# Kernel optimization log

Measured on AMD Instinct MI355X. Metric: run time of the kernel, lower is better.

Reference implementation:

```python
import jax, jax.numpy as jnp
import numpy as np

DT_RANK = 160
D_STATE = 16


def setup_inputs() -> dict:
    key = jax.random.key(0)
    ks = jax.random.split(key, 13)
    B, D, E = 32, 2560, 5120
    s = lambda k, shape, sc=0.02: (jax.random.normal(k, shape, dtype=jnp.float32) * sc)
    return {
        "x": jax.random.normal(ks[0], (1, 1, B, D), dtype=jnp.float32),
        "W_in_ssm": s(ks[1], (D, E)),
        "W_in_mlp": s(ks[2], (D, E)),
        "W_out": s(ks[3], (E, D)),
        "conv_w": s(ks[4], (4, B, E), 0.1),
        "conv_b": s(ks[5], (B, E), 0.1),
        "conv_states": jax.random.normal(ks[6], (3, 1, 1, B, E), dtype=jnp.float32),
        "Wx": s(ks[7], (E, DT_RANK + 2 * D_STATE)),
        "W_dt": s(ks[8], (DT_RANK, E)),
        "dt_bias": s(ks[9], (E,), 0.5),
        "A_log": jax.random.uniform(ks[10], (E, D_STATE), dtype=jnp.float32),
        "D": s(ks[11], (E,), 1.0),
        "h": jax.random.normal(ks[12], (B, E, D_STATE), dtype=jnp.float32) * 0.1,
    }


def reference(x, W_in_ssm, W_in_mlp, W_out, conv_w, conv_b, conv_states, Wx, W_dt, dt_bias, A_log, D, h):
    # x: [1,1,B,d_model]
    x_ssm = x @ W_in_ssm  # [1,1,B,E]
    # FIFO: 3 carried conv states + newest projection -> 4 taps
    states = jnp.concatenate([conv_states, x_ssm[None]], axis=0)  # [4,1,1,B,E]
    # unrolled 4-tap causal depthwise conv (per-batch-broadcast weights) + bias + SiLU
    conv = jnp.einsum('tabne,tne->abne', states, conv_w) + conv_b  # [1,1,B,E]
    conv = jax.nn.silu(conv)

    # --- single-step selective SSM (Mamba decode) ---
    xt = conv[0, 0]  # [B,E]
    dbc = xt @ Wx  # [B, dt_rank + 2*d_state]
    dt = jax.nn.softplus(dbc[:, :DT_RANK] @ W_dt + dt_bias)  # [B,E]
    Bm = dbc[:, DT_RANK:DT_RANK + D_STATE]  # [B,N]
    Cm = dbc[:, DT_RANK + D_STATE:]         # [B,N]
    A = -jnp.exp(A_log)                      # [E,N]
    dA = jnp.exp(dt[:, :, None] * A[None])   # [B,E,N]
    h_new = h * dA + (dt[:, :, None] * Bm[:, None, :]) * xt[:, :, None]
    y = jnp.einsum('ben,bn->be', h_new, Cm) + D * xt  # [B,E]
    y = y[None, None]  # [1,1,B,E]

    # gated residual branch: silu-activated mlp projection
    residual = jax.nn.silu(x @ W_in_mlp)  # [1,1,B,E]
    out = y * residual
    return out @ W_out  # [1,1,B,d_model]
```

## Files before the change

### kernel.cpp

```cpp
#include <hip/hip_runtime.h>
#include <math.h>

#define EE 5120
#define DD 2560
#define BB 32

__global__ __launch_bounds__(256) void k0_prep(const float* __restrict__ x,
                                               float* __restrict__ xT,
                                               float* __restrict__ dbc) {
  int g = blockIdx.x * 256 + threadIdx.x;
  if (g < BB * DD) {
    int b = g / DD, k = g % DD;
    xT[k * BB + b] = x[g];
  }
  if (g < BB * 192) dbc[g] = 0.f;
}

__global__ __launch_bounds__(256) void k1a_gemm_in(const float* __restrict__ Wssm,
                                                   const float* __restrict__ Wmlp,
                                                   const float* __restrict__ xT,
                                                   float* __restrict__ P1) {
  const int bid  = blockIdx.x;
  const int cb   = bid % 160;
  const int so   = bid / 160;
  const int lane = threadIdx.x & 63;
  const int ks   = __builtin_amdgcn_readfirstlane((int)(threadIdx.x >> 6));
  const int c    = cb * 64 + lane;
  const float* __restrict__ W = (c < EE) ? Wssm : Wmlp;
  const int e  = (c < EE) ? c : c - EE;
  const int k0 = so * 320 + ks * 80;

  float acc[BB];
#pragma unroll
  for (int b = 0; b < BB; ++b) acc[b] = 0.f;

  const float* __restrict__ wp = W + (size_t)k0 * EE + e;
  const float* __restrict__ xp = xT + k0 * BB;
  for (int kk = 0; kk < 80; kk += 4) {
    float w0 = wp[(size_t)(kk + 0) * EE];
    float w1 = wp[(size_t)(kk + 1) * EE];
    float w2 = wp[(size_t)(kk + 2) * EE];
    float w3 = wp[(size_t)(kk + 3) * EE];
#pragma unroll
    for (int b = 0; b < BB; ++b) acc[b] = fmaf(xp[(kk + 0) * BB + b], w0, acc[b]);
#pragma unroll
    for (int b = 0; b < BB; ++b) acc[b] = fmaf(xp[(kk + 1) * BB + b], w1, acc[b]);
#pragma unroll
    for (int b = 0; b < BB; ++b) acc[b] = fmaf(xp[(kk + 2) * BB + b], w2, acc[b]);
#pragma unroll
    for (int b = 0; b < BB; ++b) acc[b] = fmaf(xp[(kk + 3) * BB + b], w3, acc[b]);
  }

  __shared__ float red[4][64][17];
  const int ksid = threadIdx.x >> 6;
#pragma unroll
  for (int half = 0; half < 2; ++half) {
    __syncthreads();
#pragma unroll
    for (int i = 0; i < 16; ++i) red[ksid][lane][i] = acc[half * 16 + i];
    __syncthreads();
#pragma unroll
    for (int j = 0; j < 4; ++j) {
      int bi = ksid * 4 + j;
      float v = red[0][lane][bi] + red[1][lane][bi] +
                red[2][lane][bi] + red[3][lane][bi];
      int b = half * 16 + bi;
      P1[((size_t)(so * BB + b)) * 10240 + c] = v;
    }
  }
}

__global__ __launch_bounds__(256) void k1b_epilogue(const float* __restrict__ P1,
                                                    const float* __restrict__ cs,
                                                    const float* __restrict__ cw,
                                                    const float* __restrict__ cbv,
                                                    float* __restrict__ xt,
                                                    float* __restrict__ res) {
  int g = blockIdx.x * 256 + threadIdx.x;
  int e = g % EE;
  int b = g / EE;
  float xs = 0.f, xm = 0.f;
#pragma unroll
  for (int so = 0; so < 8; ++so) {
    xs += P1[((size_t)(so * BB + b)) * 10240 + e];
    xm += P1[((size_t)(so * BB + b)) * 10240 + EE + e];
  }
  size_t be = (size_t)b * EE + e;
  const size_t T = (size_t)BB * EE;
  float conv = cs[be] * cw[be] + cs[T + be] * cw[T + be] +
               cs[2 * T + be] * cw[2 * T + be] + xs * cw[3 * T + be] + cbv[be];
  float sig = 1.f / (1.f + expf(-conv));
  xt[be] = conv * sig;
  float sm = 1.f / (1.f + expf(-xm));
  res[be] = xm * sm;
}

__global__ __launch_bounds__(256) void k2_dbc(const float* __restrict__ xt,
                                              const float* __restrict__ Wx,
                                              float* __restrict__ dbc) {
  const int bid  = blockIdx.x;
  const int cbi  = bid % 3;
  const int so   = bid / 3;
  const int lane = threadIdx.x & 63;
  const int j    = cbi * 64 + lane;
  const int k0   = so * 80 + (int)(threadIdx.x >> 6) * 20;

  float acc[BB];
#pragma unroll
  for (int b = 0; b < BB; ++b) acc[b] = 0.f;

  for (int kk = 0; kk < 20; kk += 4) {
    int k = k0 + kk;
    float w0 = Wx[(size_t)(k + 0) * 192 + j];
    float w1 = Wx[(size_t)(k + 1) * 192 + j];
    float w2 = Wx[(size_t)(k + 2) * 192 + j];
    float w3 = Wx[(size_t)(k + 3) * 192 + j];
#pragma unroll
    for (int b = 0; b < BB; ++b) acc[b] = fmaf(xt[(size_t)b * EE + k + 0], w0, acc[b]);
#pragma unroll
    for (int b = 0; b < BB; ++b) acc[b] = fmaf(xt[(size_t)b * EE + k + 1], w1, acc[b]);
#pragma unroll
    for (int b = 0; b < BB; ++b) acc[b] = fmaf(xt[(size_t)b * EE + k + 2], w2, acc[b]);
#pragma unroll
    for (int b = 0; b < BB; ++b) acc[b] = fmaf(xt[(size_t)b * EE + k + 3], w3, acc[b]);
  }

  __shared__ float red[4][64][17];
  const int ksid = threadIdx.x >> 6;
#pragma unroll
  for (int half = 0; half < 2; ++half) {
    __syncthreads();
#pragma unroll
    for (int i = 0; i < 16; ++i) red[ksid][lane][i] = acc[half * 16 + i];
    __syncthreads();
#pragma unroll
    for (int jj = 0; jj < 4; ++jj) {
      int bi = ksid * 4 + jj;
      float v = red[0][lane][bi] + red[1][lane][bi] +
                red[2][lane][bi] + red[3][lane][bi];
      int b = half * 16 + bi;
      atomicAdd(&dbc[b * 192 + j], v);
    }
  }
}

__global__ __launch_bounds__(256) void k3_ssm(const float* __restrict__ dbc,
                                              const float* __restrict__ Wdt,
                                              const float* __restrict__ dt_bias,
                                              const float* __restrict__ A_log,
                                              const float* __restrict__ Dvec,
                                              const float* __restrict__ h,
                                              const float* __restrict__ xt,
                                              const float* __restrict__ res,
                                              float* __restrict__ zT) {
  const int eb   = blockIdx.x % 80;
  const int bg   = blockIdx.x / 80;
  const int lane = threadIdx.x & 63;
  const int sub  = __builtin_amdgcn_readfirstlane((int)(threadIdx.x >> 6));
  const int e    = eb * 64 + lane;
  const int bq   = bg * 4 + sub;
  const int b0   = bq * 2, b1 = b0 + 1;

  float a0 = 0.f, a1 = 0.f;
  const float* __restrict__ d0 = dbc + b0 * 192;
  const float* __restrict__ d1 = dbc + b1 * 192;
  for (int r = 0; r < 160; r += 4) {
    float w0 = Wdt[(size_t)(r + 0) * EE + e];
    float w1 = Wdt[(size_t)(r + 1) * EE + e];
    float w2 = Wdt[(size_t)(r + 2) * EE + e];
    float w3 = Wdt[(size_t)(r + 3) * EE + e];
    a0 = fmaf(d0[r + 0], w0, a0);  a1 = fmaf(d1[r + 0], w0, a1);
    a0 = fmaf(d0[r + 1], w1, a0);  a1 = fmaf(d1[r + 1], w1, a1);
    a0 = fmaf(d0[r + 2], w2, a0);  a1 = fmaf(d1[r + 2], w2, a1);
    a0 = fmaf(d0[r + 3], w3, a0);  a1 = fmaf(d1[r + 3], w3, a1);
  }

  float An[16];
#pragma unroll
  for (int n = 0; n < 16; ++n) An[n] = -expf(A_log[e * 16 + n]);
  const float bias = dt_bias[e];
  const float Dv = Dvec[e];

#pragma unroll
  for (int t = 0; t < 2; ++t) {
    int b = t ? b1 : b0;
    float a = t ? a1 : a0;
    float v = a + bias;
    float dt = (v > 20.f) ? v : log1pf(expf(v));
    size_t be = (size_t)b * EE + e;
    float xb = xt[be];
    const float* __restrict__ hb = h + be * 16;
    const float* __restrict__ Bm = dbc + b * 192 + 160;
    const float* __restrict__ Cm = dbc + b * 192 + 176;
    float y = 0.f;
#pragma unroll
    for (int n = 0; n < 16; ++n) {
      float dA = expf(dt * An[n]);
      float hn = fmaf(hb[n], dA, dt * Bm[n] * xb);
      y = fmaf(hn, Cm[n], y);
    }
    y = fmaf(Dv, xb, y);
    zT[e * BB + b] = y * res[be];
  }
}

__global__ __launch_bounds__(256) void k4a_gemm_out(const float* __restrict__ Wout,
                                                    const float* __restrict__ zT,
                                                    float* __restrict__ P4) {
  const int bid  = blockIdx.x;
  const int cb   = bid % 40;
  const int so   = bid / 40;
  const int lane = threadIdx.x & 63;
  const int ks   = __builtin_amdgcn_readfirstlane((int)(threadIdx.x >> 6));
  const int d    = cb * 64 + lane;
  const int k0   = so * 320 + ks * 80;

  float acc[BB];
#pragma unroll
  for (int b = 0; b < BB; ++b) acc[b] = 0.f;

  const float* __restrict__ wp = Wout + (size_t)k0 * DD + d;
  const float* __restrict__ xp = zT + k0 * BB;
  for (int kk = 0; kk < 80; kk += 4) {
    float w0 = wp[(size_t)(kk + 0) * DD];
    float w1 = wp[(size_t)(kk + 1) * DD];
    float w2 = wp[(size_t)(kk + 2) * DD];
    float w3 = wp[(size_t)(kk + 3) * DD];
#pragma unroll
    for (int b = 0; b < BB; ++b) acc[b] = fmaf(xp[(kk + 0) * BB + b], w0, acc[b]);
#pragma unroll
    for (int b = 0; b < BB; ++b) acc[b] = fmaf(xp[(kk + 1) * BB + b], w1, acc[b]);
#pragma unroll
    for (int b = 0; b < BB; ++b) acc[b] = fmaf(xp[(kk + 2) * BB + b], w2, acc[b]);
#pragma unroll
    for (int b = 0; b < BB; ++b) acc[b] = fmaf(xp[(kk + 3) * BB + b], w3, acc[b]);
  }

  __shared__ float red[4][64][17];
  const int ksid = threadIdx.x >> 6;
#pragma unroll
  for (int half = 0; half < 2; ++half) {
    __syncthreads();
#pragma unroll
    for (int i = 0; i < 16; ++i) red[ksid][lane][i] = acc[half * 16 + i];
    __syncthreads();
#pragma unroll
    for (int j = 0; j < 4; ++j) {
      int bi = ksid * 4 + j;
      float v = red[0][lane][bi] + red[1][lane][bi] +
                red[2][lane][bi] + red[3][lane][bi];
      int b = half * 16 + bi;
      P4[((size_t)(so * BB + b)) * DD + d] = v;
    }
  }
}

__global__ __launch_bounds__(256) void k4b_reduce(const float* __restrict__ P4,
                                                  float* __restrict__ out) {
  int g = blockIdx.x * 256 + threadIdx.x;
  int d = g % DD;
  int b = g / DD;
  float s = 0.f;
#pragma unroll
  for (int so = 0; so < 16; ++so) s += P4[((size_t)(so * BB + b)) * DD + d];
  out[g] = s;
}

extern "C" void kernel_launch(void* const* d_in, const int* in_sizes, int n_in,
                              void* d_out, int out_size, void* d_ws, size_t ws_size,
                              hipStream_t stream) {
  const float* x       = (const float*)d_in[0];
  const float* Wssm    = (const float*)d_in[1];
  const float* Wmlp    = (const float*)d_in[2];
  const float* Wout    = (const float*)d_in[3];
  const float* conv_w  = (const float*)d_in[4];
  const float* conv_b  = (const float*)d_in[5];
  const float* conv_st = (const float*)d_in[6];
  const float* Wx      = (const float*)d_in[7];
  const float* Wdt     = (const float*)d_in[8];
  const float* dt_bias = (const float*)d_in[9];
  const float* A_log   = (const float*)d_in[10];
  const float* Dvec    = (const float*)d_in[11];
  const float* h       = (const float*)d_in[12];
  float* out = (float*)d_out;

  float* ws = (float*)d_ws;
  float* xT  = ws;
  float* P1  = xT  + 81920;
  float* xt  = P1  + 2621440;
  float* res = xt  + 163840;
  float* dbc = res + 163840;
  float* zT  = dbc + 6144;
  float* P4  = zT  + 163840;

  hipLaunchKernelGGL(k0_prep,     dim3(320),  dim3(256), 0, stream, x, xT, dbc);
  hipLaunchKernelGGL(k1a_gemm_in, dim3(1280), dim3(256), 0, stream, Wssm, Wmlp, xT, P1);
  hipLaunchKernelGGL(k1b_epilogue,dim3(640),  dim3(256), 0, stream, P1, conv_st, conv_w, conv_b, xt, res);
  hipLaunchKernelGGL(k2_dbc,      dim3(192),  dim3(256), 0, stream, xt, Wx, dbc);
  hipLaunchKernelGGL(k3_ssm,      dim3(320),  dim3(256), 0, stream, dbc, Wdt, dt_bias, A_log, Dvec, h, xt, res, zT);
  hipLaunchKernelGGL(k4a_gemm_out,dim3(640),  dim3(256), 0, stream, Wout, zT, P4);
  hipLaunchKernelGGL(k4b_reduce,  dim3(320),  dim3(256), 0, stream, P4, out);
}
```

Measured before the change: 279.8 us.

## Unify split-K GEMMs with shared-memory activations, float2 columns and prefetched weights

The two separate split-K GEMM kernels are replaced by one generic kernel. It stages the activation slice in shared memory, gives each thread two adjacent output columns loaded as float2, and double-buffers the weight loads one step ahead. Each block now covers 128 columns instead of 64, so the block count halves while the weight stream stays about the same. The intent is to cut redundant global activation reads and raise memory-level parallelism on the weight-bandwidth-bound GEMMs. In exchange it uses more registers (64 accumulators per thread) and a 40KB shared buffer, which limits occupancy.

```diff
diff --git a/kernel.cpp b/kernel.cpp
--- a/kernel.cpp
+++ b/kernel.cpp
@@ -16,57 +16,89 @@
   if (g < BB * 192) dbc[g] = 0.f;
 }
 
-__global__ __launch_bounds__(256) void k1a_gemm_in(const float* __restrict__ Wssm,
-                                                   const float* __restrict__ Wmlp,
-                                                   const float* __restrict__ xT,
-                                                   float* __restrict__ P1) {
-  const int bid  = blockIdx.x;
-  const int cb   = bid % 160;
-  const int so   = bid / 160;
+__device__ __forceinline__ void compute4(float2* __restrict__ acc,
+                                         const float2* __restrict__ wcur,
+                                         const float* __restrict__ xw, int kk) {
+#pragma unroll
+  for (int j = 0; j < 4; ++j) {
+    const float4* __restrict__ xk = (const float4*)(xw + (kk + j) * BB);
+    float2 wj = wcur[j];
+#pragma unroll
+    for (int q = 0; q < 8; ++q) {
+      float4 xv = xk[q];
+      acc[q * 4 + 0].x = fmaf(xv.x, wj.x, acc[q * 4 + 0].x);
+      acc[q * 4 + 0].y = fmaf(xv.x, wj.y, acc[q * 4 + 0].y);
+      acc[q * 4 + 1].x = fmaf(xv.y, wj.x, acc[q * 4 + 1].x);
+      acc[q * 4 + 1].y = fmaf(xv.y, wj.y, acc[q * 4 + 1].y);
+      acc[q * 4 + 2].x = fmaf(xv.z, wj.x, acc[q * 4 + 2].x);
+      acc[q * 4 + 2].y = fmaf(xv.z, wj.y, acc[q * 4 + 2].y);
+      acc[q * 4 + 3].x = fmaf(xv.w, wj.x, acc[q * 4 + 3].x);
+      acc[q * 4 + 3].y = fmaf(xv.w, wj.y, acc[q * 4 + 3].y);
+    }
+  }
+}
+
+__global__ __launch_bounds__(256, 4) void gemm_sk(const float* __restrict__ W0,
+                                                  const float* __restrict__ W1,
+                                                  int wsplit, int wstride,
+                                                  const float* __restrict__ xsrc,
+                                                  float* __restrict__ P,
+                                                  int pstride, int ncb) {
+  __shared__ float smem[10240];
+  const int cb   = blockIdx.x % ncb;
+  const int so   = blockIdx.x / ncb;
   const int lane = threadIdx.x & 63;
-  const int ks   = __builtin_amdgcn_readfirstlane((int)(threadIdx.x >> 6));
-  const int c    = cb * 64 + lane;
-  const float* __restrict__ W = (c < EE) ? Wssm : Wmlp;
-  const int e  = (c < EE) ? c : c - EE;
-  const int k0 = so * 320 + ks * 80;
-
-  float acc[BB];
-#pragma unroll
-  for (int b = 0; b < BB; ++b) acc[b] = 0.f;
-
-  const float* __restrict__ wp = W + (size_t)k0 * EE + e;
-  const float* __restrict__ xp = xT + k0 * BB;
-  for (int kk = 0; kk < 80; kk += 4) {
-    float w0 = wp[(size_t)(kk + 0) * EE];
-    float w1 = wp[(size_t)(kk + 1) * EE];
-    float w2 = wp[(size_t)(kk + 2) * EE];
-    float w3 = wp[(size_t)(kk + 3) * EE];
-#pragma unroll
-    for (int b = 0; b < BB; ++b) acc[b] = fmaf(xp[(kk + 0) * BB + b], w0, acc[b]);
-#pragma unroll
-    for (int b = 0; b < BB; ++b) acc[b] = fmaf(xp[(kk + 1) * BB + b], w1, acc[b]);
-#pragma unroll
-    for (int b = 0; b < BB; ++b) acc[b] = fmaf(xp[(kk + 2) * BB + b], w2, acc[b]);
-#pragma unroll
-    for (int b = 0; b < BB; ++b) acc[b] = fmaf(xp[(kk + 3) * BB + b], w3, acc[b]);
-  }
-
-  __shared__ float red[4][64][17];
-  const int ksid = threadIdx.x >> 6;
-#pragma unroll
-  for (int half = 0; half < 2; ++half) {
-    __syncthreads();
-#pragma unroll
-    for (int i = 0; i < 16; ++i) red[ksid][lane][i] = acc[half * 16 + i];
-    __syncthreads();
-#pragma unroll
-    for (int j = 0; j < 4; ++j) {
-      int bi = ksid * 4 + j;
-      float v = red[0][lane][bi] + red[1][lane][bi] +
-                red[2][lane][bi] + red[3][lane][bi];
-      int b = half * 16 + bi;
-      P1[((size_t)(so * BB + b)) * 10240 + c] = v;
-    }
+  const int wv   = threadIdx.x >> 6;
+  const int ccol = cb * 128 + lane * 2;
+  const float* __restrict__ W = (ccol < wsplit) ? W0 : W1;
+  const int wc = (ccol < wsplit) ? ccol : ccol - wsplit;
+  const int k0 = so * 320;
+
+  {
+    const float4* __restrict__ src = (const float4*)(xsrc + (size_t)k0 * BB);
+    float4* __restrict__ dst = (float4*)smem;
+    for (int i = threadIdx.x; i < 2560; i += 256) dst[i] = src[i];
+  }
+  __syncthreads();
+
+  float2 acc[32];
+#pragma unroll
+  for (int b = 0; b < 32; ++b) acc[b] = make_float2(0.f, 0.f);
+
+  const int kw = wv * 80;
+  const float* __restrict__ wp = W + (size_t)(k0 + kw) * wstride + wc;
+  const float* __restrict__ xw = smem + kw * BB;
+
+  float2 wb[4];
+#pragma unroll
+  for (int p = 0; p < 4; ++p) wb[p] = *(const float2*)(wp + (size_t)p * wstride);
+
+  for (int kk = 0; kk < 76; kk += 4) {
+    float2 wcur[4];
+#pragma unroll
+    for (int p = 0; p < 4; ++p) wcur[p] = wb[p];
+#pragma unroll
+    for (int p = 0; p < 4; ++p)
+      wb[p] = *(const float2*)(wp + (size_t)(kk + 4 + p) * wstride);
+    compute4(acc, wcur, xw, kk);
+  }
+  compute4(acc, wb, xw, 76);
+
+#pragma unroll 1
+  for (int p = 0; p < 8; ++p) {
+    __syncthreads();
+#pragma unroll
+    for (int q = 0; q < 4; ++q) {
+      smem[(wv * 64 + lane) * 9 + q * 2 + 0] = acc[p * 4 + q].x;
+      smem[(wv * 64 + lane) * 9 + q * 2 + 1] = acc[p * 4 + q].y;
+    }
+    __syncthreads();
+    float sx = smem[(0 * 64 + lane) * 9 + wv * 2] + smem[(1 * 64 + lane) * 9 + wv * 2] +
+               smem[(2 * 64 + lane) * 9 + wv * 2] + smem[(3 * 64 + lane) * 9 + wv * 2];
+    float sy = smem[(0 * 64 + lane) * 9 + wv * 2 + 1] + smem[(1 * 64 + lane) * 9 + wv * 2 + 1] +
+               smem[(2 * 64 + lane) * 9 + wv * 2 + 1] + smem[(3 * 64 + lane) * 9 + wv * 2 + 1];
+    int b = p * 4 + wv;
+    *(float2*)&P[((size_t)(so * BB + b)) * pstride + ccol] = make_float2(sx, sy);
   }
 }
 
@@ -201,57 +233,6 @@
     }
     y = fmaf(Dv, xb, y);
     zT[e * BB + b] = y * res[be];
-  }
-}
-
-__global__ __launch_bounds__(256) void k4a_gemm_out(const float* __restrict__ Wout,
-                                                    const float* __restrict__ zT,
-                                                    float* __restrict__ P4) {
-  const int bid  = blockIdx.x;
-  const int cb   = bid % 40;
-  const int so   = bid / 40;
-  const int lane = threadIdx.x & 63;
-  const int ks   = __builtin_amdgcn_readfirstlane((int)(threadIdx.x >> 6));
-  const int d    = cb * 64 + lane;
-  const int k0   = so * 320 + ks * 80;
-
-  float acc[BB];
-#pragma unroll
-  for (int b = 0; b < BB; ++b) acc[b] = 0.f;
-
-  const float* __restrict__ wp = Wout + (size_t)k0 * DD + d;
-  const float* __restrict__ xp = zT + k0 * BB;
-  for (int kk = 0; kk < 80; kk += 4) {
-    float w0 = wp[(size_t)(kk + 0) * DD];
-    float w1 = wp[(size_t)(kk + 1) * DD];
-    float w2 = wp[(size_t)(kk + 2) * DD];
-    float w3 = wp[(size_t)(kk + 3) * DD];
-#pragma unroll
-    for (int b = 0; b < BB; ++b) acc[b] = fmaf(xp[(kk + 0) * BB + b], w0, acc[b]);
-#pragma unroll
-    for (int b = 0; b < BB; ++b) acc[b] = fmaf(xp[(kk + 1) * BB + b], w1, acc[b]);
-#pragma unroll
-    for (int b = 0; b < BB; ++b) acc[b] = fmaf(xp[(kk + 2) * BB + b], w2, acc[b]);
-#pragma unroll
-    for (int b = 0; b < BB; ++b) acc[b] = fmaf(xp[(kk + 3) * BB + b], w3, acc[b]);
-  }
-
-  __shared__ float red[4][64][17];
-  const int ksid = threadIdx.x >> 6;
-#pragma unroll
-  for (int half = 0; half < 2; ++half) {
-    __syncthreads();
-#pragma unroll
-    for (int i = 0; i < 16; ++i) red[ksid][lane][i] = acc[half * 16 + i];
-    __syncthreads();
-#pragma unroll
-    for (int j = 0; j < 4; ++j) {
-      int bi = ksid * 4 + j;
-      float v = red[0][lane][bi] + red[1][lane][bi] +
-                red[2][lane][bi] + red[3][lane][bi];
-      int b = half * 16 + bi;
-      P4[((size_t)(so * BB + b)) * DD + d] = v;
-    }
   }
 }
 
@@ -294,10 +275,12 @@
   float* P4  = zT  + 163840;
 
   hipLaunchKernelGGL(k0_prep,     dim3(320),  dim3(256), 0, stream, x, xT, dbc);
-  hipLaunchKernelGGL(k1a_gemm_in, dim3(1280), dim3(256), 0, stream, Wssm, Wmlp, xT, P1);
+  hipLaunchKernelGGL(gemm_sk,     dim3(640),  dim3(256), 0, stream,
+                     Wssm, Wmlp, EE, EE, xT, P1, 10240, 80);
   hipLaunchKernelGGL(k1b_epilogue,dim3(640),  dim3(256), 0, stream, P1, conv_st, conv_w, conv_b, xt, res);
   hipLaunchKernelGGL(k2_dbc,      dim3(192),  dim3(256), 0, stream, xt, Wx, dbc);
   hipLaunchKernelGGL(k3_ssm,      dim3(320),  dim3(256), 0, stream, dbc, Wdt, dt_bias, A_log, Dvec, h, xt, res, zT);
-  hipLaunchKernelGGL(k4a_gemm_out,dim3(640),  dim3(256), 0, stream, Wout, zT, P4);
+  hipLaunchKernelGGL(gemm_sk,     dim3(320),  dim3(256), 0, stream,
+                     Wout, Wout, 1 << 30, DD, zT, P4, DD, 20);
   hipLaunchKernelGGL(k4b_reduce,  dim3(320),  dim3(256), 0, stream, P4, out);
 }
```

Result: slower. 378.4 us (+35.2%).
